# Performance work log

Hardware: AMD Instinct MI355X
Metric: run time of the kernel (lower is better)

The kernel has to match this reference:

```python
import jax, jax.numpy as jnp
import numpy as np

N_NODES = 100000
N_EDGES = 1600000
IN_FEATS = 256
OUT_FEATS = 128


def setup_inputs() -> dict:
    key = jax.random.key(0)
    k1, k2, k3, k4 = jax.random.split(key, 4)
    feat = jax.random.normal(k1, (N_NODES, IN_FEATS), dtype=jnp.float32)
    W = jax.random.normal(k2, (IN_FEATS, OUT_FEATS), dtype=jnp.float32)
    src = jax.random.randint(k3, (N_EDGES,), 0, N_NODES, dtype=jnp.int64)
    dst = jax.random.randint(k4, (N_EDGES,), 0, N_NODES, dtype=jnp.int64)
    return {"feat": feat, "W": W, "src": src, "dst": dst}


def reference(feat, W, src, dst):
    # h_self = feat @ W  -> [N, out_feats]
    h_self = feat @ W
    # update_all(copy_src('h','m'), sum('m','neigh')): gather source features,
    # scatter-sum at destination nodes (SpMM over the edge list).
    msgs = h_self[src]                                        # [E, out_feats]
    h_neigh = jax.ops.segment_sum(msgs, dst, num_segments=N_NODES)
    # in-degree per node
    degs = jax.ops.segment_sum(jnp.ones(dst.shape, jnp.float32), dst,
                               num_segments=N_NODES)          # [N]
    rst = (h_neigh + h_self) / (degs[:, None] + 1.0)
    return jax.nn.relu(rst)
```

## Files before the change

kernel.cpp:

```cpp
#include <hip/hip_runtime.h>
#include <hip/hip_bf16.h>


#define IN_FEATS 256
#define OUT_FEATS 128
#define NUM_NODES 100000
#define NUM_EDGES 1600000

#define NB 782
#define EC 128
#define CHUNK_E 12500
#define BCAP 3072
#define GEMM_BLOCKS 391

typedef __attribute__((ext_vector_type(8))) short short8;
typedef __attribute__((ext_vector_type(8))) unsigned short ushort8;
typedef __attribute__((ext_vector_type(4))) float f32x4;

static __device__ inline unsigned short f2bfu(float x) {
    union { __hip_bfloat16 h; unsigned short u; } c;
    c.h = __float2bfloat16(x);
    return c.u;
}
static __device__ inline ushort2 f2bfu2(float x, float y) {
    union { __hip_bfloat162 h; ushort2 u; } c;
    c.h = __float22bfloat162_rn(make_float2(x, y));
    return c.u;
}
static __device__ inline float bf2f(unsigned short h) {
    return __uint_as_float((unsigned)h << 16);
}

__global__ __launch_bounds__(256) void convert_hist(
    const float* __restrict__ W, unsigned short* __restrict__ Wt,
    const int* __restrict__ dst, int* __restrict__ counts)
{
    int b = blockIdx.x;
    int t = threadIdx.x;
    if (b < 128) {
        int i = b * 256 + t;
        int n = i >> 8;
        int k = i & 255;
        Wt[i] = f2bfu(W[(size_t)k * OUT_FEATS + n]);
        return;
    }
    int c = b - 128;
    __shared__ int hist[NB];
    for (int i = t; i < NB; i += 256) hist[i] = 0;
    __syncthreads();
    const int4* dp = (const int4*)(dst + c * CHUNK_E);
    for (int i = t; i < CHUNK_E / 4; i += 256) {
        int4 d4 = dp[i];
        atomicAdd(&hist[d4.x >> 7], 1);
        atomicAdd(&hist[d4.y >> 7], 1);
        atomicAdd(&hist[d4.z >> 7], 1);
        atomicAdd(&hist[d4.w >> 7], 1);
    }
    __syncthreads();
    for (int i = t; i < NB; i += 256) counts[c * NB + i] = hist[i];
}

__global__ __launch_bounds__(128) void scan_chunks(
    int* __restrict__ counts, int* __restrict__ bucket_total)
{
    __shared__ int sd[128];
    int b = blockIdx.x, t = threadIdx.x;
    int v = counts[t * NB + b];
    sd[t] = v;
    __syncthreads();
    for (int o = 1; o < 128; o <<= 1) {
        int x = (t >= o) ? sd[t - o] : 0;
        __syncthreads();
        sd[t] += x;
        __syncthreads();
    }
    counts[t * NB + b] = sd[t] - v;
    if (t == 127) bucket_total[b] = sd[127];
}

__global__ __launch_bounds__(256) void scan_buckets(
    const int* __restrict__ bucket_total, int* __restrict__ bucket_base)
{
    __shared__ int sd[256];
    int t = threadIdx.x;
    int base = t * 4;
    int v0 = 0, v1 = 0, v2 = 0, v3 = 0;
    if (base + 3 < NB) {
        int4 v = *(const int4*)&bucket_total[base];
        v0 = v.x; v1 = v.y; v2 = v.z; v3 = v.w;
    } else {
        if (base + 0 < NB) v0 = bucket_total[base + 0];
        if (base + 1 < NB) v1 = bucket_total[base + 1];
        if (base + 2 < NB) v2 = bucket_total[base + 2];
        if (base + 3 < NB) v3 = bucket_total[base + 3];
    }
    int s = v0 + v1 + v2 + v3;
    sd[t] = s;
    __syncthreads();
    for (int o = 1; o < 256; o <<= 1) {
        int x = (t >= o) ? sd[t - o] : 0;
        __syncthreads();
        sd[t] += x;
        __syncthreads();
    }
    int e0 = sd[t] - s, e1 = e0 + v0, e2 = e1 + v1, e3 = e2 + v2;
    if (base + 0 < NB) bucket_base[base + 0] = e0;
    if (base + 1 < NB) bucket_base[base + 1] = e1;
    if (base + 2 < NB) bucket_base[base + 2] = e2;
    if (base + 3 < NB) bucket_base[base + 3] = e3;
}

__global__ __launch_bounds__(512) void scatter_k(
    const int* __restrict__ src, const int* __restrict__ dst,
    const int* __restrict__ counts, const int* __restrict__ bucket_base,
    int* __restrict__ bedges)
{
    __shared__ int cur[NB];
    const int tid = threadIdx.x;
    int c = blockIdx.x;
    for (int i = tid; i < NB; i += 512)
        cur[i] = bucket_base[i] + counts[c * NB + i];
    __syncthreads();
    const int4* dp = (const int4*)(dst + c * CHUNK_E);
    const int4* sp = (const int4*)(src + c * CHUNK_E);
    for (int i = tid; i < CHUNK_E / 4; i += 512) {
        int4 d4 = dp[i];
        int4 s4 = sp[i];
        int dv[4] = { d4.x, d4.y, d4.z, d4.w };
        int sv[4] = { s4.x, s4.y, s4.z, s4.w };
#pragma unroll
        for (int j = 0; j < 4; ++j) {
            int d = dv[j];
            int slot = atomicAdd(&cur[d >> 7], 1);
            bedges[slot] = sv[j] | ((d & 127) << 17);
        }
    }
}

static __device__ inline void stage_chunk(
    const float* __restrict__ feat, char* smem, int buf,
    int bm0, int k0, int t, int M)
{
#pragma unroll
    for (int j = 0; j < 4; ++j) {
        int G = j * 512 + t;
        int r = G >> 3;
        int g = G & 7;
        int srow = bm0 + r;
        if (srow > M - 1) srow = M - 1;
        const float* src = feat + (size_t)srow * IN_FEATS + k0 + ((g ^ (r & 7)) << 2);
        __builtin_amdgcn_global_load_lds(
            (const __attribute__((address_space(1))) unsigned int*)src,
            (__attribute__((address_space(3))) unsigned int*)(smem + buf * 32768 + G * 16),
            16, 0, 0);
    }
}

__global__ __launch_bounds__(512, 4) void gemm_k(
    const float* __restrict__ feat, const unsigned short* __restrict__ Wt,
    unsigned short* __restrict__ hself16, int M)
{
    __shared__ char smem_raw[65536];
    const int tid = threadIdx.x;

    const int w  = tid >> 6;
    const int l  = tid & 63;
    const int lf = l & 15;
    const int lg = (l >> 4) & 3;
    const int bm0 = blockIdx.x * 256;

    f32x4 acc[2][8];
#pragma unroll
    for (int mt = 0; mt < 2; ++mt)
#pragma unroll
        for (int nt = 0; nt < 8; ++nt)
            acc[mt][nt] = (f32x4){0.f, 0.f, 0.f, 0.f};

    stage_chunk(feat, smem_raw, 0, bm0, 0, tid, M);
    __syncthreads();

#pragma unroll
    for (int kc = 0; kc < 8; ++kc) {
        const int buf = kc & 1;
        if (kc < 7)
            stage_chunk(feat, smem_raw, buf ^ 1, bm0, (kc + 1) * 32, tid, M);

        const int k8 = kc * 4;

        short8 af[2];
#pragma unroll
        for (int mt = 0; mt < 2; ++mt) {
            int r  = w * 32 + mt * 16 + lf;
            int rs = r & 7;
            const char* base = smem_raw + buf * 32768 + r * 128;
            float4 f0 = *(const float4*)(base + ((((lg << 1) + 0) ^ rs) << 4));
            float4 f1 = *(const float4*)(base + ((((lg << 1) + 1) ^ rs) << 4));
            ushort2 c0 = f2bfu2(f0.x, f0.y);
            ushort2 c1 = f2bfu2(f0.z, f0.w);
            ushort2 c2 = f2bfu2(f1.x, f1.y);
            ushort2 c3 = f2bfu2(f1.z, f1.w);
            af[mt] = (short8){ (short)c0.x, (short)c0.y, (short)c1.x, (short)c1.y,
                               (short)c2.x, (short)c2.y, (short)c3.x, (short)c3.y };
        }

#pragma unroll
        for (int nh = 0; nh < 2; ++nh) {
            short8 bf[4];
#pragma unroll
            for (int q = 0; q < 4; ++q) {
                int nt = nh * 4 + q;
                int n = nt * 16 + lf;
                bf[q] = *(const short8*)(Wt + (size_t)n * IN_FEATS + (k8 + lg) * 8);
            }
#pragma unroll
            for (int q = 0; q < 4; ++q) {
                int nt = nh * 4 + q;
                acc[0][nt] = __builtin_amdgcn_mfma_f32_16x16x32_bf16(af[0], bf[q], acc[0][nt], 0, 0, 0);
                acc[1][nt] = __builtin_amdgcn_mfma_f32_16x16x32_bf16(af[1], bf[q], acc[1][nt], 0, 0, 0);
            }
        }

        __syncthreads();
    }

    unsigned short* ep = (unsigned short*)smem_raw;
#pragma unroll
    for (int mt = 0; mt < 2; ++mt)
#pragma unroll
        for (int nt = 0; nt < 8; ++nt)
#pragma unroll
            for (int r = 0; r < 4; ++r) {
                int row = w * 32 + mt * 16 + lg * 4 + r;
                ep[row * 128 + nt * 16 + lf] = f2bfu(acc[mt][nt][r]);
            }
    __syncthreads();
#pragma unroll
    for (int i = 0; i < 8; ++i) {
        int lrow = w * 32 + i * 4 + (l >> 4);
        ushort8 v = *(const ushort8*)(ep + lrow * 128 + (l & 15) * 8);
        int grow = bm0 + lrow;
        if (grow < M)
            *(ushort8*)(hself16 + (size_t)grow * OUT_FEATS + (l & 15) * 8) = v;
    }
}

__global__ __launch_bounds__(512, 8) void sort_k(
    const int* __restrict__ bucket_base, const int* __restrict__ bucket_total,
    int* __restrict__ bedges, int* __restrict__ nodeinfo)
{
    __shared__ int sorted[BCAP];
    __shared__ int cnt[128], off[128], cursor[128], sd[128];

    int b = blockIdx.x, t = threadIdx.x;
    int base = bucket_base[b];
    int tot = bucket_total[b];
    if (tot > BCAP) tot = BCAP;

    if (t < 128) cnt[t] = 0;
    __syncthreads();
    for (int i = t; i < tot; i += 512)
        atomicAdd(&cnt[bedges[base + i] >> 17], 1);
    __syncthreads();
    if (t < 128) sd[t] = cnt[t];
    __syncthreads();
    for (int o = 1; o < 128; o <<= 1) {
        int x = 0;
        if (t < 128 && t >= o) x = sd[t - o];
        __syncthreads();
        if (t < 128) sd[t] += x;
        __syncthreads();
    }
    if (t < 128) { int e = sd[t] - cnt[t]; off[t] = e; cursor[t] = e; }
    __syncthreads();
    for (int i = t; i < tot; i += 512) {
        int e = bedges[base + i];
        int r = atomicAdd(&cursor[e >> 17], 1);
        sorted[r] = e & 0x1FFFF;
    }
    __syncthreads();
    for (int i = t; i < tot; i += 512)
        bedges[base + i] = sorted[i];
    if (t < 128)
        nodeinfo[b * 128 + t] = (off[t] << 16) | cnt[t];
}

__global__ __launch_bounds__(512, 4) void gather_k(
    const int* __restrict__ bucket_base, const int* __restrict__ bucket_total,
    const int* __restrict__ bedges, const int* __restrict__ nodeinfo,
    const unsigned short* __restrict__ hself16, float* __restrict__ out)
{
    __shared__ int sorted[BCAP];
    int b = blockIdx.x, t = threadIdx.x;
    int base = bucket_base[b];
    int tot = bucket_total[b];
    if (tot > BCAP) tot = BCAP;
    int nnodes = NUM_NODES - b * 128;
    if (nnodes > 128) nnodes = 128;

    for (int i = t; i < tot; i += 512)
        sorted[i] = bedges[base + i];
    __syncthreads();

    const int gid = t >> 4;
    const int lf  = t & 15;

#pragma unroll
    for (int rep = 0; rep < 4; ++rep) {
        int ln = rep * 32 + gid;
        if (ln >= nnodes) continue;
        int info = nodeinfo[b * 128 + ln];
        int beg = info >> 16;
        int cn  = info & 0xFFFF;
        int end = beg + cn;
        int n = b * 128 + ln;
        ushort8 hs = *(const ushort8*)(hself16 + (size_t)n * OUT_FEATS + lf * 8);

        float acc[8];
#pragma unroll
        for (int i = 0; i < 8; ++i) acc[i] = 0.f;

        for (int j0 = beg; j0 < end; j0 += 8) {
            int  ss[8];
            bool pp[8];
#pragma unroll
            for (int q = 0; q < 8; ++q) {
                int jj = j0 + q;
                pp[q] = jj < end;
                ss[q] = pp[q] ? sorted[jj] : 0;
            }
            ushort8 h[8];
#pragma unroll
            for (int q = 0; q < 8; ++q)
                h[q] = *(const ushort8*)(hself16 + (size_t)ss[q] * OUT_FEATS + lf * 8);
#pragma unroll
            for (int q = 0; q < 8; ++q)
                if (pp[q]) {
#pragma unroll
                    for (int i = 0; i < 8; ++i) acc[i] += bf2f(h[q][i]);
                }
        }

        float inv = 1.0f / (float)(cn + 1);
        float v[8];
#pragma unroll
        for (int i = 0; i < 8; ++i)
            v[i] = fmaxf((acc[i] + bf2f(hs[i])) * inv, 0.f);
        float4* op = (float4*)(out + (size_t)n * OUT_FEATS + lf * 8);
        op[0] = make_float4(v[0], v[1], v[2], v[3]);
        op[1] = make_float4(v[4], v[5], v[6], v[7]);
    }
}

extern "C" void kernel_launch(void* const* d_in, const int* in_sizes, int n_in,
                              void* d_out, int out_size, void* d_ws, size_t ws_size,
                              hipStream_t stream) {
    const float* feat = (const float*)d_in[0];
    const float* W    = (const float*)d_in[1];
    const int*   src  = (const int*)d_in[2];
    const int*   dst  = (const int*)d_in[3];
    float* out = (float*)d_out;

    char* ws = (char*)d_ws;
    unsigned short* hself16 = (unsigned short*)ws;
    unsigned short* Wt      = (unsigned short*)(ws + 25600000);
    int* counts       = (int*)(ws + 25665536);
    int* bucket_total = (int*)(ws + 26065920);
    int* bucket_base  = (int*)(ws + 26069120);
    int* bedges       = (int*)(ws + 26072320);
    int* nodeinfo     = counts;

    convert_hist<<<256, 256, 0, stream>>>(W, Wt, dst, counts);
    scan_chunks<<<NB, 128, 0, stream>>>(counts, bucket_total);
    scan_buckets<<<1, 256, 0, stream>>>(bucket_total, bucket_base);
    scatter_k<<<EC, 512, 0, stream>>>(src, dst, counts, bucket_base, bedges);
    gemm_k<<<GEMM_BLOCKS, 512, 0, stream>>>(feat, Wt, hself16, NUM_NODES);
    sort_k<<<NB, 512, 0, stream>>>(bucket_base, bucket_total, bedges, nodeinfo);
    gather_k<<<NB, 512, 0, stream>>>(bucket_base, bucket_total, bedges, nodeinfo,
                                     hself16, out);
}
```

Baseline: 297.2 us.

## Triple-buffer GEMM staging with register-prefetched W and fuse sort into gather

```diff
diff --git a/kernel.cpp b/kernel.cpp
--- a/kernel.cpp
+++ b/kernel.cpp
@@ -11,7 +11,7 @@
 #define EC 128
 #define CHUNK_E 12500
 #define BCAP 3072
-#define GEMM_BLOCKS 391
+#define GEMM_BLOCKS 782
 
 typedef __attribute__((ext_vector_type(8))) short short8;
 typedef __attribute__((ext_vector_type(8))) unsigned short ushort8;
@@ -137,13 +137,13 @@
     }
 }
 
-static __device__ inline void stage_chunk(
+static __device__ __forceinline__ void stage_chunk(
     const float* __restrict__ feat, char* smem, int buf,
     int bm0, int k0, int t, int M)
 {
 #pragma unroll
     for (int j = 0; j < 4; ++j) {
-        int G = j * 512 + t;
+        int G = j * 256 + t;
         int r = G >> 3;
         int g = G & 7;
         int srow = bm0 + r;
@@ -151,23 +151,65 @@
         const float* src = feat + (size_t)srow * IN_FEATS + k0 + ((g ^ (r & 7)) << 2);
         __builtin_amdgcn_global_load_lds(
             (const __attribute__((address_space(1))) unsigned int*)src,
-            (__attribute__((address_space(3))) unsigned int*)(smem + buf * 32768 + G * 16),
+            (__attribute__((address_space(3))) unsigned int*)(smem + buf * 16384 + G * 16),
             16, 0, 0);
     }
 }
 
-__global__ __launch_bounds__(512, 4) void gemm_k(
+template<int KC>
+static __device__ __forceinline__ void gemm_step(
+    const float* __restrict__ feat, const unsigned short* __restrict__ Wt,
+    char* smem_raw, f32x4 (&acc)[2][8], short8 (&bf)[8],
+    int w32, int lf, int lg, int bm0, int tid, int M)
+{
+    asm volatile("s_waitcnt vmcnt(%0)" :: "n"((KC == 7) ? 8 : 12) : "memory");
+    __builtin_amdgcn_s_barrier();
+    __builtin_amdgcn_sched_barrier(0);
+
+    short8 af[2];
+#pragma unroll
+    for (int mt = 0; mt < 2; ++mt) {
+        int r  = w32 + mt * 16 + lf;
+        int rs = r & 7;
+        const char* base = smem_raw + (KC % 3) * 16384 + r * 128;
+        float4 f0 = *(const float4*)(base + ((((lg << 1) + 0) ^ rs) << 4));
+        float4 f1 = *(const float4*)(base + ((((lg << 1) + 1) ^ rs) << 4));
+        ushort2 c0 = f2bfu2(f0.x, f0.y);
+        ushort2 c1 = f2bfu2(f0.z, f0.w);
+        ushort2 c2 = f2bfu2(f1.x, f1.y);
+        ushort2 c3 = f2bfu2(f1.z, f1.w);
+        af[mt] = (short8){ (short)c0.x, (short)c0.y, (short)c1.x, (short)c1.y,
+                           (short)c2.x, (short)c2.y, (short)c3.x, (short)c3.y };
+    }
+
+#pragma unroll
+    for (int q = 0; q < 8; ++q) {
+        acc[0][q] = __builtin_amdgcn_mfma_f32_16x16x32_bf16(af[0], bf[q], acc[0][q], 0, 0, 0);
+        acc[1][q] = __builtin_amdgcn_mfma_f32_16x16x32_bf16(af[1], bf[q], acc[1][q], 0, 0, 0);
+    }
+
+    if (KC < 7) {
+#pragma unroll
+        for (int q = 0; q < 8; ++q)
+            bf[q] = *(const short8*)(Wt + (size_t)(q * 16 + lf) * IN_FEATS
+                                        + ((KC + 1) * 4 + lg) * 8);
+    }
+    if (KC < 6)
+        stage_chunk(feat, smem_raw, (KC + 2) % 3, bm0, (KC + 2) * 32, tid, M);
+}
+
+__global__ __launch_bounds__(256, 2) void gemm_k(
     const float* __restrict__ feat, const unsigned short* __restrict__ Wt,
     unsigned short* __restrict__ hself16, int M)
 {
-    __shared__ char smem_raw[65536];
+    __shared__ char smem_raw[49152];
     const int tid = threadIdx.x;
-
-    const int w  = tid >> 6;
-    const int l  = tid & 63;
-    const int lf = l & 15;
-    const int lg = (l >> 4) & 3;
-    const int bm0 = blockIdx.x * 256;
+    const int w   = tid >> 6;
+    const int l   = tid & 63;
+    const int lf  = l & 15;
+    const int lg  = (l >> 4) & 3;
+    const int w32 = w * 32;
+    const int bm0 = blockIdx.x * 128;
 
     f32x4 acc[2][8];
 #pragma unroll
@@ -176,53 +218,25 @@
         for (int nt = 0; nt < 8; ++nt)
             acc[mt][nt] = (f32x4){0.f, 0.f, 0.f, 0.f};
 
+    short8 bf[8];
     stage_chunk(feat, smem_raw, 0, bm0, 0, tid, M);
-    __syncthreads();
-
-#pragma unroll
-    for (int kc = 0; kc < 8; ++kc) {
-        const int buf = kc & 1;
-        if (kc < 7)
-            stage_chunk(feat, smem_raw, buf ^ 1, bm0, (kc + 1) * 32, tid, M);
-
-        const int k8 = kc * 4;
-
-        short8 af[2];
-#pragma unroll
-        for (int mt = 0; mt < 2; ++mt) {
-            int r  = w * 32 + mt * 16 + lf;
-            int rs = r & 7;
-            const char* base = smem_raw + buf * 32768 + r * 128;
-            float4 f0 = *(const float4*)(base + ((((lg << 1) + 0) ^ rs) << 4));
-            float4 f1 = *(const float4*)(base + ((((lg << 1) + 1) ^ rs) << 4));
-            ushort2 c0 = f2bfu2(f0.x, f0.y);
-            ushort2 c1 = f2bfu2(f0.z, f0.w);
-            ushort2 c2 = f2bfu2(f1.x, f1.y);
-            ushort2 c3 = f2bfu2(f1.z, f1.w);
-            af[mt] = (short8){ (short)c0.x, (short)c0.y, (short)c1.x, (short)c1.y,
-                               (short)c2.x, (short)c2.y, (short)c3.x, (short)c3.y };
-        }
-
-#pragma unroll
-        for (int nh = 0; nh < 2; ++nh) {
-            short8 bf[4];
-#pragma unroll
-            for (int q = 0; q < 4; ++q) {
-                int nt = nh * 4 + q;
-                int n = nt * 16 + lf;
-                bf[q] = *(const short8*)(Wt + (size_t)n * IN_FEATS + (k8 + lg) * 8);
-            }
-#pragma unroll
-            for (int q = 0; q < 4; ++q) {
-                int nt = nh * 4 + q;
-                acc[0][nt] = __builtin_amdgcn_mfma_f32_16x16x32_bf16(af[0], bf[q], acc[0][nt], 0, 0, 0);
-                acc[1][nt] = __builtin_amdgcn_mfma_f32_16x16x32_bf16(af[1], bf[q], acc[1][nt], 0, 0, 0);
-            }
-        }
-
-        __syncthreads();
-    }
-
+    asm volatile("" ::: "memory");
+#pragma unroll
+    for (int q = 0; q < 8; ++q)
+        bf[q] = *(const short8*)(Wt + (size_t)(q * 16 + lf) * IN_FEATS + lg * 8);
+    asm volatile("" ::: "memory");
+    stage_chunk(feat, smem_raw, 1, bm0, 32, tid, M);
+
+    gemm_step<0>(feat, Wt, smem_raw, acc, bf, w32, lf, lg, bm0, tid, M);
+    gemm_step<1>(feat, Wt, smem_raw, acc, bf, w32, lf, lg, bm0, tid, M);
+    gemm_step<2>(feat, Wt, smem_raw, acc, bf, w32, lf, lg, bm0, tid, M);
+    gemm_step<3>(feat, Wt, smem_raw, acc, bf, w32, lf, lg, bm0, tid, M);
+    gemm_step<4>(feat, Wt, smem_raw, acc, bf, w32, lf, lg, bm0, tid, M);
+    gemm_step<5>(feat, Wt, smem_raw, acc, bf, w32, lf, lg, bm0, tid, M);
+    gemm_step<6>(feat, Wt, smem_raw, acc, bf, w32, lf, lg, bm0, tid, M);
+    gemm_step<7>(feat, Wt, smem_raw, acc, bf, w32, lf, lg, bm0, tid, M);
+
+    __syncthreads();
     unsigned short* ep = (unsigned short*)smem_raw;
 #pragma unroll
     for (int mt = 0; mt < 2; ++mt)
@@ -230,13 +244,13 @@
         for (int nt = 0; nt < 8; ++nt)
 #pragma unroll
             for (int r = 0; r < 4; ++r) {
-                int row = w * 32 + mt * 16 + lg * 4 + r;
+                int row = w32 + mt * 16 + lg * 4 + r;
                 ep[row * 128 + nt * 16 + lf] = f2bfu(acc[mt][nt][r]);
             }
     __syncthreads();
 #pragma unroll
     for (int i = 0; i < 8; ++i) {
-        int lrow = w * 32 + i * 4 + (l >> 4);
+        int lrow = w32 + i * 4 + (l >> 4);
         ushort8 v = *(const ushort8*)(ep + lrow * 128 + (l & 15) * 8);
         int grow = bm0 + lrow;
         if (grow < M)
@@ -244,52 +258,14 @@
     }
 }
 
-__global__ __launch_bounds__(512, 8) void sort_k(
+__global__ __launch_bounds__(512, 4) void sort_gather(
     const int* __restrict__ bucket_base, const int* __restrict__ bucket_total,
-    int* __restrict__ bedges, int* __restrict__ nodeinfo)
+    const int* __restrict__ bedges, const unsigned short* __restrict__ hself16,
+    float* __restrict__ out)
 {
     __shared__ int sorted[BCAP];
     __shared__ int cnt[128], off[128], cursor[128], sd[128];
 
-    int b = blockIdx.x, t = threadIdx.x;
-    int base = bucket_base[b];
-    int tot = bucket_total[b];
-    if (tot > BCAP) tot = BCAP;
-
-    if (t < 128) cnt[t] = 0;
-    __syncthreads();
-    for (int i = t; i < tot; i += 512)
-        atomicAdd(&cnt[bedges[base + i] >> 17], 1);
-    __syncthreads();
-    if (t < 128) sd[t] = cnt[t];
-    __syncthreads();
-    for (int o = 1; o < 128; o <<= 1) {
-        int x = 0;
-        if (t < 128 && t >= o) x = sd[t - o];
-        __syncthreads();
-        if (t < 128) sd[t] += x;
-        __syncthreads();
-    }
-    if (t < 128) { int e = sd[t] - cnt[t]; off[t] = e; cursor[t] = e; }
-    __syncthreads();
-    for (int i = t; i < tot; i += 512) {
-        int e = bedges[base + i];
-        int r = atomicAdd(&cursor[e >> 17], 1);
-        sorted[r] = e & 0x1FFFF;
-    }
-    __syncthreads();
-    for (int i = t; i < tot; i += 512)
-        bedges[base + i] = sorted[i];
-    if (t < 128)
-        nodeinfo[b * 128 + t] = (off[t] << 16) | cnt[t];
-}
-
-__global__ __launch_bounds__(512, 4) void gather_k(
-    const int* __restrict__ bucket_base, const int* __restrict__ bucket_total,
-    const int* __restrict__ bedges, const int* __restrict__ nodeinfo,
-    const unsigned short* __restrict__ hself16, float* __restrict__ out)
-{
-    __shared__ int sorted[BCAP];
     int b = blockIdx.x, t = threadIdx.x;
     int base = bucket_base[b];
     int tot = bucket_total[b];
@@ -297,8 +273,27 @@
     int nnodes = NUM_NODES - b * 128;
     if (nnodes > 128) nnodes = 128;
 
+    if (t < 128) cnt[t] = 0;
+    __syncthreads();
     for (int i = t; i < tot; i += 512)
-        sorted[i] = bedges[base + i];
+        atomicAdd(&cnt[bedges[base + i] >> 17], 1);
+    __syncthreads();
+    if (t < 128) sd[t] = cnt[t];
+    __syncthreads();
+    for (int o = 1; o < 128; o <<= 1) {
+        int x = 0;
+        if (t < 128 && t >= o) x = sd[t - o];
+        __syncthreads();
+        if (t < 128) sd[t] += x;
+        __syncthreads();
+    }
+    if (t < 128) { int e = sd[t] - cnt[t]; off[t] = e; cursor[t] = e; }
+    __syncthreads();
+    for (int i = t; i < tot; i += 512) {
+        int e = bedges[base + i];
+        int r = atomicAdd(&cursor[e >> 17], 1);
+        sorted[r] = e & 0x1FFFF;
+    }
     __syncthreads();
 
     const int gid = t >> 4;
@@ -308,9 +303,8 @@
     for (int rep = 0; rep < 4; ++rep) {
         int ln = rep * 32 + gid;
         if (ln >= nnodes) continue;
-        int info = nodeinfo[b * 128 + ln];
-        int beg = info >> 16;
-        int cn  = info & 0xFFFF;
+        int beg = off[ln];
+        int cn  = cnt[ln];
         int end = beg + cn;
         int n = b * 128 + ln;
         ushort8 hs = *(const ushort8*)(hself16 + (size_t)n * OUT_FEATS + lf * 8);
@@ -367,14 +361,12 @@
     int* bucket_total = (int*)(ws + 26065920);
     int* bucket_base  = (int*)(ws + 26069120);
     int* bedges       = (int*)(ws + 26072320);
-    int* nodeinfo     = counts;
 
     convert_hist<<<256, 256, 0, stream>>>(W, Wt, dst, counts);
     scan_chunks<<<NB, 128, 0, stream>>>(counts, bucket_total);
     scan_buckets<<<1, 256, 0, stream>>>(bucket_total, bucket_base);
     scatter_k<<<EC, 512, 0, stream>>>(src, dst, counts, bucket_base, bedges);
-    gemm_k<<<GEMM_BLOCKS, 512, 0, stream>>>(feat, Wt, hself16, NUM_NODES);
-    sort_k<<<NB, 512, 0, stream>>>(bucket_base, bucket_total, bedges, nodeinfo);
-    gather_k<<<NB, 512, 0, stream>>>(bucket_base, bucket_total, bedges, nodeinfo,
-                                     hself16, out);
-}
+    gemm_k<<<GEMM_BLOCKS, 256, 0, stream>>>(feat, Wt, hself16, NUM_NODES);
+    sort_gather<<<NB, 512, 0, stream>>>(bucket_base, bucket_total, bedges,
+                                        hself16, out);
+}
```

After: 293.0 us. Within noise of the previous version (-1.4%).
